# Optimization experiments

Measured on AMD Instinct MI355X. Metric: run time of the kernel, lower is better.

## Reference

```python
import jax, jax.numpy as jnp
import numpy as np

H = 16      # q heads
G = 4       # groups (n_rep)
THETA = 10000.0


def _rope(x, cos, sin):
    # x pairs adjacent elements (torch complex view of reshape(..., -1, 2))
    x0 = x[..., ::2]
    x1 = x[..., 1::2]
    r0 = x0 * cos - x1 * sin
    r1 = x0 * sin + x1 * cos
    return jnp.stack([r0, r1], axis=-1).reshape(x.shape)


def setup_inputs() -> dict:
    key = jax.random.key(0)
    ks = jax.random.split(key, 5)
    B, S, D = 2, 2048, 1024
    return {
        "x": jax.random.normal(ks[0], (B, S, D), jnp.float32),
        "Wq": jax.random.normal(ks[1], (D, D), jnp.float32) * 0.02,
        "Wk": jax.random.normal(ks[2], (D, D // G), jnp.float32) * 0.02,
        "Wv": jax.random.normal(ks[3], (D, D // G), jnp.float32) * 0.02,
        "Wo": jax.random.normal(ks[4], (D, D), jnp.float32) * 0.02,
    }


def reference(x, Wq, Wk, Wv, Wo):
    B, S, D = x.shape
    hd = D // H                     # head dim = 64
    Hkv = H // G                    # kv heads = 4

    q = x @ Wq                      # (B,S,D)
    k = x @ Wk                      # (B,S,D/G)
    v = x @ Wv                      # (B,S,D/G)

    # repeat_kv: (B,S,Hkv,hd) -> (B,S,H,hd)
    k = jnp.repeat(k.reshape(B, S, Hkv, hd), G, axis=2)
    v = jnp.repeat(v.reshape(B, S, Hkv, hd), G, axis=2)

    # RoPE angles: freqs precomputed over hidden_dim (as in source)
    inv = 1.0 / (THETA ** (jnp.arange(0, D, 2, dtype=jnp.float32) / D))  # (D/2,)
    ang = jnp.arange(S, dtype=jnp.float32)[:, None] * inv[None, :]       # (S,D/2)
    q = _rope(q, jnp.cos(ang)[None], jnp.sin(ang)[None])                 # (B,S,D)
    angk = ang[:, : hd // 2]                                             # (S,hd/2)
    k = _rope(k, jnp.cos(angk)[None, :, None, :], jnp.sin(angk)[None, :, None, :])

    q = q.reshape(B, S, H, hd).transpose(0, 2, 1, 3)   # (B,H,S,hd)
    k = k.transpose(0, 2, 1, 3)
    v = v.transpose(0, 2, 1, 3)

    # NOTE: scale uses sqrt(hidden_dim), faithful to source
    scores = jnp.einsum('bhqd,bhkd->bhqk', q, k) / jnp.sqrt(jnp.float32(D))
    p = jax.nn.softmax(scores, axis=-1)
    o = jnp.einsum('bhqk,bhkd->bhqd', p, v)
    o = o.transpose(0, 2, 1, 3).reshape(B, S, D)
    return o @ Wo
```

## Files before the change

### kernel.cpp

```cpp
#include <hip/hip_runtime.h>
#include <math.h>

#define BATCH 2
#define SEQ   2048
#define DMODEL 1024
#define KDIM  1024
#define NH    16
#define HDIM  64
#define GRP   4
#define NKV   4

enum { M_PLAIN = 0, M_QKV = 1 };

#define LN_THETA 9.210340371976184f

typedef short bf8_t __attribute__((ext_vector_type(8)));
typedef float f4_t __attribute__((ext_vector_type(4)));
typedef unsigned short us4_t __attribute__((ext_vector_type(4)));
typedef unsigned short us8_t __attribute__((ext_vector_type(8)));

#define QB_OFF 0
#define KB_OFF 4194304
#define VB_OFF (4194304 + 1048576)

__device__ __forceinline__ unsigned short f2bf(float f) {
  unsigned int u = __float_as_uint(f);
  u += 0x7fffu + ((u >> 16) & 1u);
  return (unsigned short)(u >> 16);
}

__device__ __forceinline__ void gload_lds16(const void* g, void* l) {
  typedef __attribute__((address_space(1))) unsigned int gu32;
  typedef __attribute__((address_space(3))) unsigned int lu32;
  __builtin_amdgcn_global_load_lds((const gu32*)g, (lu32*)l, 16, 0, 0);
}

__global__ __launch_bounds__(256) void conv_x(const float* __restrict__ in,
                                              unsigned short* __restrict__ out) {
  const int i = blockIdx.x * 256 + threadIdx.x;
  float4 v = ((const float4*)in)[i];
  us4_t o = {f2bf(v.x), f2bf(v.y), f2bf(v.z), f2bf(v.w)};
  ((us4_t*)out)[i] = o;
}

__global__ __launch_bounds__(256) void convT(const float* __restrict__ W,
                                             unsigned short* __restrict__ out,
                                             int N, int rowoff) {
  __shared__ unsigned short T[64][72];
  const int t = threadIdx.x;
  const int k0 = blockIdx.y * 64, n0 = blockIdx.x * 64;
  const int kr = t >> 4, n4 = (t & 15) * 4;
#pragma unroll
  for (int i = 0; i < 4; ++i) {
    const int k = kr + i * 16;
    float4 v = *(const float4*)&W[(size_t)(k0 + k) * N + n0 + n4];
    T[n4 + 0][k] = f2bf(v.x);
    T[n4 + 1][k] = f2bf(v.y);
    T[n4 + 2][k] = f2bf(v.z);
    T[n4 + 3][k] = f2bf(v.w);
  }
  __syncthreads();
#pragma unroll
  for (int i = 0; i < 2; ++i) {
    const int c = t + i * 256;
    const int n = c >> 3, kc = (c & 7) * 8;
    us8_t v = *(const us8_t*)&T[n][kc];
    *(us8_t*)&out[(size_t)(rowoff + n0 + n) * KDIM + k0 + kc] = v;
  }
}

template <int MODE>
__global__ __launch_bounds__(256, 3) void gemm_bf16(const unsigned short* __restrict__ A,
                                                    const unsigned short* __restrict__ Bt,
                                                    void* __restrict__ Cdst_, int N) {
  __shared__ __align__(16) unsigned short As[64 * 64];
  __shared__ __align__(16) unsigned short Bs[128 * 64];

  const int tid = threadIdx.x;
  const int lane = tid & 63, quad = lane >> 4, l16 = lane & 15;
  const int w = tid >> 6, wm = w >> 1, wn = w & 1;
  const int row0 = blockIdx.x * 64, col0 = blockIdx.y * 128;

  const int m0 = tid >> 2;
  const int kc0 = (tid & 3) ^ ((m0 >> 1) & 3);
  const unsigned short* Ag0 = A + (size_t)(row0 + m0) * KDIM + kc0 * 8;
  const unsigned short* Bg0 = Bt + (size_t)(col0 + m0) * KDIM + kc0 * 8;
  unsigned short* Al0 = &As[tid * 8];
  unsigned short* Bl0 = &Bs[tid * 8];

  int aoff[2][2], boff[4][2];
#pragma unroll
  for (int mi = 0; mi < 2; ++mi) {
    const int am = wm * 32 + mi * 16 + l16;
    const int sw = quad ^ ((am >> 1) & 3);
#pragma unroll
    for (int kh = 0; kh < 2; ++kh)
      aoff[mi][kh] = kh * 2048 + (((am << 2) | sw) << 3);
  }
#pragma unroll
  for (int ni = 0; ni < 4; ++ni) {
    const int bn = wn * 64 + ni * 16 + l16;
    const int sw = quad ^ ((bn >> 1) & 3);
#pragma unroll
    for (int kh = 0; kh < 2; ++kh)
      boff[ni][kh] = kh * 4096 + (((bn << 2) | sw) << 3);
  }

  f4_t acc[2][4];
#pragma unroll
  for (int mi = 0; mi < 2; ++mi)
#pragma unroll
    for (int ni = 0; ni < 4; ++ni) acc[mi][ni] = (f4_t){0.f, 0.f, 0.f, 0.f};

  for (int kb = 0; kb < KDIM; kb += 64) {
    __syncthreads();
    gload_lds16(Ag0 + kb,       Al0);
    gload_lds16(Ag0 + kb + 32,  Al0 + 2048);
    gload_lds16(Bg0 + kb,                     Bl0);
    gload_lds16(Bg0 + (size_t)64 * KDIM + kb, Bl0 + 2048);
    gload_lds16(Bg0 + kb + 32,                     Bl0 + 4096);
    gload_lds16(Bg0 + (size_t)64 * KDIM + kb + 32, Bl0 + 6144);
    __syncthreads();

    bf8_t af[2][2], bfr[4][2];
#pragma unroll
    for (int mi = 0; mi < 2; ++mi)
#pragma unroll
      for (int kh = 0; kh < 2; ++kh) af[mi][kh] = *(const bf8_t*)&As[aoff[mi][kh]];
#pragma unroll
    for (int ni = 0; ni < 4; ++ni)
#pragma unroll
      for (int kh = 0; kh < 2; ++kh) bfr[ni][kh] = *(const bf8_t*)&Bs[boff[ni][kh]];
#pragma unroll
    for (int kh = 0; kh < 2; ++kh)
#pragma unroll
      for (int mi = 0; mi < 2; ++mi)
#pragma unroll
        for (int ni = 0; ni < 4; ++ni)
          acc[mi][ni] = __builtin_amdgcn_mfma_f32_16x16x32_bf16(af[mi][kh], bfr[ni][kh], acc[mi][ni], 0, 0, 0);
  }

  if constexpr (MODE == M_PLAIN) {
    float* out = (float*)Cdst_;
#pragma unroll
    for (int mi = 0; mi < 2; ++mi) {
      const int rowb = row0 + wm * 32 + mi * 16 + quad * 4;
#pragma unroll
      for (int ni = 0; ni < 4; ++ni) {
        const int n = col0 + wn * 64 + ni * 16 + l16;
#pragma unroll
        for (int r = 0; r < 4; ++r)
          out[(size_t)(rowb + r) * N + n] = acc[mi][ni][r];
      }
    }
  } else {
    unsigned short* Qb = (unsigned short*)Cdst_;
    unsigned short* Kb = Qb + (KB_OFF - QB_OFF);
    unsigned short* Vb = Qb + (VB_OFF - QB_OFF);
#pragma unroll
    for (int ni = 0; ni < 4; ++ni) {
      const int nb = col0 + wn * 64 + ni * 16;
      const int n = nb + l16;
      if (nb < 1024) {
        const float inv = expf(-(float)(2 * (n >> 1)) * (LN_THETA / (float)DMODEL));
        const float sgn = (n & 1) ? 1.f : -1.f;
        const int h = n >> 6, d = n & 63;
#pragma unroll
        for (int mi = 0; mi < 2; ++mi) {
          const int rowb = row0 + wm * 32 + mi * 16 + quad * 4;
#pragma unroll
          for (int r = 0; r < 4; ++r) {
            const int row = rowb + r;
            const int bb = row >> 11, s = row & (SEQ - 1);
            const float v = acc[mi][ni][r];
            const float p = __shfl_xor(v, 1);
            float sn, cs;
            sincosf((float)s * inv, &sn, &cs);
            const float res = (v * cs + sgn * p * sn) * 0.03125f;
            Qb[((size_t)(bb * NH + h) * SEQ + s) * HDIM + d] = f2bf(res);
          }
        }
      } else if (nb < 1280) {
        const int nk = n - 1024;
        const int hkv = nk >> 6, d = nk & 63;
        const float inv = expf(-(float)(2 * (d >> 1)) * (LN_THETA / (float)DMODEL));
        const float sgn = (nk & 1) ? 1.f : -1.f;
#pragma unroll
        for (int mi = 0; mi < 2; ++mi) {
          const int rowb = row0 + wm * 32 + mi * 16 + quad * 4;
#pragma unroll
          for (int r = 0; r < 4; ++r) {
            const int row = rowb + r;
            const int bb = row >> 11, s = row & (SEQ - 1);
            const float v = acc[mi][ni][r];
            const float p = __shfl_xor(v, 1);
            float sn, cs;
            sincosf((float)s * inv, &sn, &cs);
            const float res = v * cs + sgn * p * sn;
            Kb[((size_t)(bb * NKV + hkv) * SEQ + s) * HDIM + d] = f2bf(res);
          }
        }
      } else {
        const int nv = n - 1280;
        const int hkv = nv >> 6, d = nv & 63;
#pragma unroll
        for (int mi = 0; mi < 2; ++mi) {
          const int s0 = row0 + wm * 32 + mi * 16 + quad * 4;
          const int bb = s0 >> 11, s = s0 & (SEQ - 1);
          us4_t st = {f2bf(acc[mi][ni][0]), f2bf(acc[mi][ni][1]),
                      f2bf(acc[mi][ni][2]), f2bf(acc[mi][ni][3])};
          *(us4_t*)&Vb[((size_t)(bb * NKV + hkv) * HDIM + d) * SEQ + s] = st;
        }
      }
    }
  }
}

__global__ __launch_bounds__(256, 2) void attn_fwd(const unsigned short* __restrict__ Q,
                                                   const unsigned short* __restrict__ K,
                                                   const unsigned short* __restrict__ V,
                                                   unsigned short* __restrict__ O) {
  __shared__ __align__(16) unsigned short Kt[4096];
  __shared__ __align__(16) unsigned short Vt[4096];
  __shared__ __align__(16) unsigned short Pt[4][2048];

  const int b = blockIdx.x >> 4;
  const int h = blockIdx.x & (NH - 1);
  const int hkv = h >> 2;
  const int q0 = blockIdx.y * 128;
  const int tid = threadIdx.x;
  const int w = tid >> 6;
  const int lane = tid & 63;
  const int quad = lane >> 4;
  const int l16 = lane & 15;

  const unsigned short* Qg = Q + ((size_t)(b * NH + h) * SEQ + q0 + w * 32) * HDIM;
  const unsigned short* Kg = K + (size_t)(b * NKV + hkv) * SEQ * HDIM;
  const unsigned short* Vg = V + (size_t)(b * NKV + hkv) * HDIM * SEQ;

  bf8_t qb[2][2];
#pragma unroll
  for (int g = 0; g < 2; ++g)
#pragma unroll
    for (int half = 0; half < 2; ++half)
      qb[g][half] = *(const bf8_t*)(Qg + (size_t)(g * 16 + l16) * HDIM + half * 32 + quad * 8);

  bf8_t ones;
#pragma unroll
  for (int i = 0; i < 8; ++i) ones[i] = (short)0x3F80;

  f4_t accO[2][4];
#pragma unroll
  for (int g = 0; g < 2; ++g)
#pragma unroll
    for (int d = 0; d < 4; ++d) accO[g][d] = (f4_t){0.f, 0.f, 0.f, 0.f};
  f4_t accL[2] = {(f4_t){0.f, 0.f, 0.f, 0.f}, (f4_t){0.f, 0.f, 0.f, 0.f}};

  const int x7 = l16 & 7;
  const int kc0 = (quad ^ x7) << 3;
  const int kc1 = kc0 ^ 32;
  unsigned short* Ptw = Pt[w];

  const int srow = tid >> 3;
  const int sch = tid & 7;

  for (int k0 = 0; k0 < SEQ; k0 += 64) {
    __syncthreads();
#pragma unroll
    for (int i = 0; i < 2; ++i) {
      const int row = srow + i * 32;
      const int pcol = ((sch ^ (row & 7)) << 3);
      *(bf8_t*)&Kt[row * 64 + pcol] = *(const bf8_t*)(Kg + (size_t)(k0 + row) * HDIM + sch * 8);
      *(bf8_t*)&Vt[row * 64 + pcol] = *(const bf8_t*)(Vg + (size_t)row * SEQ + k0 + sch * 8);
    }
    __syncthreads();

#pragma unroll
    for (int cb = 0; cb < 4; ++cb) {
      const int krow = (cb * 16 + l16) * 64;
      bf8_t kf0 = *(const bf8_t*)&Kt[krow + kc0];
      bf8_t kf1 = *(const bf8_t*)&Kt[krow + kc1];
      const int pcol = (((cb * 2 + (quad >> 1)) ^ x7) << 3) + ((quad & 1) << 2);
#pragma unroll
      for (int g = 0; g < 2; ++g) {
        f4_t s = (f4_t){0.f, 0.f, 0.f, 0.f};
        s = __builtin_amdgcn_mfma_f32_16x16x32_bf16(kf0, qb[g][0], s, 0, 0, 0);
        s = __builtin_amdgcn_mfma_f32_16x16x32_bf16(kf1, qb[g][1], s, 0, 0, 0);
        us4_t p = {f2bf(__expf(s[0])), f2bf(__expf(s[1])),
                   f2bf(__expf(s[2])), f2bf(__expf(s[3]))};
        *(us4_t*)&Ptw[(g * 16 + l16) * 64 + pcol] = p;
      }
    }

    bf8_t pa[2][2];
#pragma unroll
    for (int g = 0; g < 2; ++g) {
      const int prow = (g * 16 + l16) * 64;
      pa[g][0] = *(const bf8_t*)&Ptw[prow + kc0];
      pa[g][1] = *(const bf8_t*)&Ptw[prow + kc1];
      accL[g] = __builtin_amdgcn_mfma_f32_16x16x32_bf16(pa[g][0], ones, accL[g], 0, 0, 0);
      accL[g] = __builtin_amdgcn_mfma_f32_16x16x32_bf16(pa[g][1], ones, accL[g], 0, 0, 0);
    }

#pragma unroll
    for (int db = 0; db < 4; ++db) {
      const int vrow = (db * 16 + l16) * 64;
      bf8_t vf0 = *(const bf8_t*)&Vt[vrow + kc0];
      bf8_t vf1 = *(const bf8_t*)&Vt[vrow + kc1];
#pragma unroll
      for (int g = 0; g < 2; ++g) {
        accO[g][db] = __builtin_amdgcn_mfma_f32_16x16x32_bf16(pa[g][0], vf0, accO[g][db], 0, 0, 0);
        accO[g][db] = __builtin_amdgcn_mfma_f32_16x16x32_bf16(pa[g][1], vf1, accO[g][db], 0, 0, 0);
      }
    }
  }

#pragma unroll
  for (int g = 0; g < 2; ++g)
#pragma unroll
    for (int r = 0; r < 4; ++r) {
      const float linv = 1.0f / accL[g][r];
      const int q = q0 + w * 32 + g * 16 + quad * 4 + r;
      unsigned short* op = O + (((size_t)b * SEQ + q) * NH + h) * HDIM;
#pragma unroll
      for (int db = 0; db < 4; ++db)
        op[db * 16 + l16] = f2bf(accO[g][db][r] * linv);
    }
}

extern "C" void kernel_launch(void* const* d_in, const int* in_sizes, int n_in,
                              void* d_out, int out_size, void* d_ws, size_t ws_size,
                              hipStream_t stream) {
  (void)in_sizes; (void)n_in; (void)out_size; (void)ws_size;
  const float* x  = (const float*)d_in[0];
  const float* Wq = (const float*)d_in[1];
  const float* Wk = (const float*)d_in[2];
  const float* Wv = (const float*)d_in[3];
  const float* Wo = (const float*)d_in[4];
  float* out = (float*)d_out;

  unsigned short* Qb    = (unsigned short*)d_ws;
  unsigned short* Kb    = Qb + 4194304;
  unsigned short* Vb    = Kb + 1048576;
  unsigned short* xb    = Vb + 1048576;
  unsigned short* Owb   = xb + 4194304;
  unsigned short* Wqkvt = Owb + 4194304;
  unsigned short* Wot   = Wqkvt + 1572864;

  dim3 blk(256);
  conv_x<<<dim3(4096), blk, 0, stream>>>(x, xb);
  convT<<<dim3(16, 16), blk, 0, stream>>>(Wq, Wqkvt, DMODEL, 0);
  convT<<<dim3(4, 16), blk, 0, stream>>>(Wk, Wqkvt, DMODEL / GRP, 1024);
  convT<<<dim3(4, 16), blk, 0, stream>>>(Wv, Wqkvt, DMODEL / GRP, 1280);
  convT<<<dim3(16, 16), blk, 0, stream>>>(Wo, Wot, DMODEL, 0);

  gemm_bf16<M_QKV><<<dim3(64, 12), blk, 0, stream>>>(xb, Wqkvt, Qb, 1536);
  attn_fwd<<<dim3(BATCH * NH, SEQ / 128), blk, 0, stream>>>(Qb, Kb, Vb, Owb);
  gemm_bf16<M_PLAIN><<<dim3(64, 8), blk, 0, stream>>>(Owb, Wot, out, DMODEL);
}
```

Before: 199.7 us.

## Split attention over key range and merge partial outputs in separate kernel

Splits the attention key loop into two halves across a new grid dimension, writing unnormalized fp32 partial outputs and row sums to workspace. A new merge kernel sums the partials, normalizes, and converts to bf16. Launch bounds are raised to 4 blocks per SM. The aim is more parallelism and occupancy (512 blocks became 1024), at the cost of extra fp32 global traffic and another kernel launch. The merge relies on there being no running max, which is why the partials can simply be added.

```diff
diff --git a/kernel.cpp b/kernel.cpp
--- a/kernel.cpp
+++ b/kernel.cpp
@@ -9,6 +9,7 @@
 #define HDIM  64
 #define GRP   4
 #define NKV   4
+#define NSPLIT 2
 
 enum { M_PLAIN = 0, M_QKV = 1 };
 
@@ -216,10 +217,11 @@
   }
 }
 
-__global__ __launch_bounds__(256, 2) void attn_fwd(const unsigned short* __restrict__ Q,
+__global__ __launch_bounds__(256, 4) void attn_fwd(const unsigned short* __restrict__ Q,
                                                    const unsigned short* __restrict__ K,
                                                    const unsigned short* __restrict__ V,
-                                                   unsigned short* __restrict__ O) {
+                                                   float* __restrict__ Opart,
+                                                   float* __restrict__ Lpart) {
   __shared__ __align__(16) unsigned short Kt[4096];
   __shared__ __align__(16) unsigned short Vt[4096];
   __shared__ __align__(16) unsigned short Pt[4][2048];
@@ -228,6 +230,7 @@
   const int h = blockIdx.x & (NH - 1);
   const int hkv = h >> 2;
   const int q0 = blockIdx.y * 128;
+  const int sp = blockIdx.z;
   const int tid = threadIdx.x;
   const int w = tid >> 6;
   const int lane = tid & 63;
@@ -264,7 +267,9 @@
   const int srow = tid >> 3;
   const int sch = tid & 7;
 
-  for (int k0 = 0; k0 < SEQ; k0 += 64) {
+  const int kbeg = sp * (SEQ / NSPLIT);
+  const int kend = kbeg + SEQ / NSPLIT;
+  for (int k0 = kbeg; k0 < kend; k0 += 64) {
     __syncthreads();
 #pragma unroll
     for (int i = 0; i < 2; ++i) {
@@ -315,17 +320,34 @@
     }
   }
 
+  float* Osp = Opart + (size_t)sp * BATCH * SEQ * NH * HDIM;
+  float* Lsp = Lpart + (size_t)sp * BATCH * SEQ * NH;
 #pragma unroll
   for (int g = 0; g < 2; ++g)
 #pragma unroll
     for (int r = 0; r < 4; ++r) {
-      const float linv = 1.0f / accL[g][r];
       const int q = q0 + w * 32 + g * 16 + quad * 4 + r;
-      unsigned short* op = O + (((size_t)b * SEQ + q) * NH + h) * HDIM;
+      const size_t rowi = ((size_t)b * SEQ + q) * NH + h;
+      float* op = Osp + rowi * HDIM;
 #pragma unroll
       for (int db = 0; db < 4; ++db)
-        op[db * 16 + l16] = f2bf(accO[g][db][r] * linv);
-    }
+        op[db * 16 + l16] = accO[g][db][r];
+      if (l16 == 0) Lsp[rowi] = accL[g][r];
+    }
+}
+
+__global__ __launch_bounds__(256) void attn_merge(const float* __restrict__ Opart,
+                                                  const float* __restrict__ Lpart,
+                                                  unsigned short* __restrict__ Ow) {
+  const int idx = blockIdx.x * 256 + threadIdx.x;
+  const int g = idx >> 4, j = (idx & 15) * 4;
+  const size_t nq = (size_t)BATCH * SEQ * NH;
+  float4 o0 = *(const float4*)&Opart[(size_t)g * HDIM + j];
+  float4 o1 = *(const float4*)&Opart[nq * HDIM + (size_t)g * HDIM + j];
+  const float il = 1.0f / (Lpart[g] + Lpart[nq + g]);
+  us4_t o = {f2bf((o0.x + o1.x) * il), f2bf((o0.y + o1.y) * il),
+             f2bf((o0.z + o1.z) * il), f2bf((o0.w + o1.w) * il)};
+  *(us4_t*)&Ow[(size_t)g * HDIM + j] = o;
 }
 
 extern "C" void kernel_launch(void* const* d_in, const int* in_sizes, int n_in,
@@ -346,6 +368,8 @@
   unsigned short* Owb   = xb + 4194304;
   unsigned short* Wqkvt = Owb + 4194304;
   unsigned short* Wot   = Wqkvt + 1572864;
+  float* Opart = (float*)(Wot + 1048576);
+  float* Lpart = Opart + (size_t)NSPLIT * 4194304;
 
   dim3 blk(256);
   conv_x<<<dim3(4096), blk, 0, stream>>>(x, xb);
@@ -355,6 +379,7 @@
   convT<<<dim3(16, 16), blk, 0, stream>>>(Wo, Wot, DMODEL, 0);
 
   gemm_bf16<M_QKV><<<dim3(64, 12), blk, 0, stream>>>(xb, Wqkvt, Qb, 1536);
-  attn_fwd<<<dim3(BATCH * NH, SEQ / 128), blk, 0, stream>>>(Qb, Kb, Vb, Owb);
+  attn_fwd<<<dim3(BATCH * NH, SEQ / 128, NSPLIT), blk, 0, stream>>>(Qb, Kb, Vb, Opart, Lpart);
+  attn_merge<<<dim3(4096), blk, 0, stream>>>(Opart, Lpart, Owb);
   gemm_bf16<M_PLAIN><<<dim3(64, 8), blk, 0, stream>>>(Owb, Wot, out, DMODEL);
 }
```

After: 185.5 us. 1.08x faster.
